# Kernel tuning notes

Hardware: AMD Instinct MI355X
Metric: run time of the kernel (lower is better)

## Reference

```python
import jax, jax.numpy as jnp
import numpy as np

B, S, HID = 2, 2048, 2048
H, KV, D = 16, 4, 128
EPS = 1e-6


def rms_norm(x, w, eps=EPS):
    # Qwen3.5 convention: (1 + weight) * RMSNorm(x), weight init 0
    v = jnp.mean(x * x, axis=-1, keepdims=True)
    return (1.0 + w) * (x * jax.lax.rsqrt(v + eps))


def rotate_half(x):
    x1, x2 = jnp.split(x, 2, axis=-1)
    return jnp.concatenate([-x2, x1], axis=-1)


def apply_rope(x, cos, sin):
    # x: [B,S,h,D]; cos/sin: [S,D]
    c = cos[None, :, None, :]
    s = sin[None, :, None, :]
    return x * c + rotate_half(x) * s


def setup_inputs():
    key = jax.random.key(0)
    ks = jax.random.split(key, 8)
    sc = 0.02
    hidden_states = jax.random.normal(ks[0], (B, S, HID), jnp.float32)
    past_key_value = jnp.zeros((B, 2, KV, S, D), jnp.float32)
    pos = jnp.arange(S, dtype=jnp.float32)
    inv_freq = 1.0 / (10000.0 ** (jnp.arange(0, D, 2, dtype=jnp.float32) / D))
    ang = pos[:, None] * inv_freq[None, :]                    # [S, D/2]
    cos = jnp.concatenate([jnp.cos(ang), jnp.cos(ang)], -1)   # [S, D]
    sin = jnp.concatenate([jnp.sin(ang), jnp.sin(ang)], -1)
    rope_rotary_cos_sin = jnp.stack([cos, sin], axis=1)       # [S, 2, D]
    context_lengths = jnp.full((B,), S, dtype=jnp.int32)
    kvcache_start_index = jnp.zeros((B,), dtype=jnp.int32)
    Wq = jax.random.normal(ks[1], (HID, H * D * 2), jnp.float32) * sc
    Wk = jax.random.normal(ks[2], (HID, KV * D), jnp.float32) * sc
    Wv = jax.random.normal(ks[3], (HID, KV * D), jnp.float32) * sc
    Wo = jax.random.normal(ks[4], (H * D, HID), jnp.float32) * sc
    q_norm_w = jax.random.normal(ks[5], (D,), jnp.float32) * sc
    k_norm_w = jax.random.normal(ks[6], (D,), jnp.float32) * sc
    return {"hidden_states": hidden_states, "past_key_value": past_key_value,
            "rope_rotary_cos_sin": rope_rotary_cos_sin,
            "context_lengths": context_lengths,
            "kvcache_start_index": kvcache_start_index,
            "Wq": Wq, "Wk": Wk, "Wv": Wv, "Wo": Wo,
            "q_norm_w": q_norm_w, "k_norm_w": k_norm_w}


def reference(hidden_states, past_key_value, rope_rotary_cos_sin,
              context_lengths, kvcache_start_index,
              Wq, Wk, Wv, Wo, q_norm_w, k_norm_w):
    # projections
    q_out = jnp.einsum('bsc,cd->bsd', hidden_states, Wq).reshape(B, S, H, 2 * D)
    query, gate = jnp.split(q_out, 2, axis=-1)                # each [B,S,H,D]
    k = jnp.einsum('bsc,cd->bsd', hidden_states, Wk).reshape(B, S, KV, D)
    v = jnp.einsum('bsc,cd->bsd', hidden_states, Wv).reshape(B, S, KV, D)
    # per-head QK RMSNorm
    query = rms_norm(query, q_norm_w)
    k = rms_norm(k, k_norm_w)
    # RoPE
    cos, sin = rope_rotary_cos_sin[:, 0, :], rope_rotary_cos_sin[:, 1, :]
    query = apply_rope(query, cos, sin)
    k = apply_rope(k, cos, sin)
    # write KV cache (prefill at start index 0)
    present = past_key_value.at[:, 0, :, :S, :].set(jnp.transpose(k, (0, 2, 1, 3)))
    present = present.at[:, 1, :, :S, :].set(jnp.transpose(v, (0, 2, 1, 3)))
    # GQA causal attention
    group = H // KV
    k_r = jnp.repeat(k, group, axis=2)                        # [B,S,H,D]
    v_r = jnp.repeat(v, group, axis=2)
    scores = jnp.einsum('bqhd,bkhd->bhqk', query, k_r) / jnp.sqrt(jnp.float32(D))
    causal = jnp.tril(jnp.ones((S, S), dtype=bool))
    scores = jnp.where(causal[None, None], scores, jnp.float32(-1e30))
    probs = jax.nn.softmax(scores, axis=-1)
    attn = jnp.einsum('bhqk,bkhd->bqhd', probs, v_r)          # [B,S,H,D]
    # sigmoid gating + output proj
    attn = attn * jax.nn.sigmoid(gate)
    out = jnp.einsum('bsd,dc->bsc', attn.reshape(B, S, H * D), Wo)
    return out, present
```

## Files before the change

kernel.cpp:

```cpp
#include <hip/hip_runtime.h>
#include <hip/hip_bf16.h>
#include <cstdint>
#include <cstddef>

#define BB   2
#define SS   2048
#define HIDD 2048
#define HH   16
#define KVH  4
#define DD   128
#define NQKV 5120
#define MM   4096

typedef unsigned short u16t;
typedef __attribute__((ext_vector_type(8))) short s16x8;
typedef __attribute__((ext_vector_type(4))) short s16x4;
typedef __attribute__((ext_vector_type(4))) float f32x4;

__device__ __forceinline__ u16t f2bf(float f) {
  unsigned u = __float_as_uint(f);
  u += 0x7fffu + ((u >> 16) & 1u);
  return (u16t)(u >> 16);
}
__device__ __forceinline__ float bf2f(u16t h) {
  return __uint_as_float(((unsigned)h) << 16);
}
__device__ __forceinline__ void gload_lds16(const void* g, void* l) {
  __builtin_amdgcn_global_load_lds(
      (const __attribute__((address_space(1))) unsigned int*)g,
      (__attribute__((address_space(3))) unsigned int*)l, 16, 0, 0);
}
__device__ __forceinline__ unsigned cvtpk_bf16(float lo, float hi) {
  unsigned r;
  asm("v_cvt_pk_bf16_f32 %0, %1, %2" : "=v"(r) : "v"(lo), "v"(hi));
  return r;
}
__device__ __forceinline__ f32x4 fmax4(f32x4 a, f32x4 b) {
  f32x4 r;
  r[0] = fmaxf(a[0], b[0]); r[1] = fmaxf(a[1], b[1]);
  r[2] = fmaxf(a[2], b[2]); r[3] = fmaxf(a[3], b[3]);
  return r;
}

__global__ __launch_bounds__(256) void prep_all(const float* __restrict__ hidden,
                                                const float* __restrict__ Wq,
                                                const float* __restrict__ Wk,
                                                const float* __restrict__ Wv,
                                                const float* __restrict__ Wo,
                                                u16t* __restrict__ Xb,
                                                u16t* __restrict__ Wt,
                                                u16t* __restrict__ Wot) {
  __shared__ float lds[64 * 65];
  int bid = blockIdx.x;
  int t = threadIdx.x;
  if (bid < 8192) {
    size_t i = ((size_t)bid * 256 + t) * 4;
    f32x4 v = *(const f32x4*)(hidden + i);
    s16x4 o;
    o[0] = (short)f2bf(v[0]); o[1] = (short)f2bf(v[1]);
    o[2] = (short)f2bf(v[2]); o[3] = (short)f2bf(v[3]);
    *(s16x4*)(Xb + i) = o;
    return;
  }
  bid -= 8192;
  const float* src; u16t* dst; int N;
  if (bid < 2048)      { src = Wq; dst = Wt;                         N = 4096; }
  else if (bid < 2304) { src = Wk; dst = Wt + (size_t)4096 * HIDD;   N = 512;  bid -= 2048; }
  else if (bid < 2560) { src = Wv; dst = Wt + (size_t)4608 * HIDD;   N = 512;  bid -= 2304; }
  else                 { src = Wo; dst = Wot;                        N = 2048; bid -= 2560; }
  const int ktiles = HIDD / 64;
  int n0 = (bid / ktiles) << 6;
  int k0 = (bid % ktiles) << 6;
#pragma unroll
  for (int i = 0; i < 16; i++) {
    int idx = i * 256 + t;
    int r = idx >> 6, c = idx & 63;
    lds[c * 65 + r] = src[(size_t)(k0 + r) * N + n0 + c];
  }
  __syncthreads();
#pragma unroll
  for (int i = 0; i < 16; i++) {
    int idx = i * 256 + t;
    int rr = idx >> 6, kk = idx & 63;
    dst[(size_t)(n0 + rr) * HIDD + k0 + kk] = f2bf(lds[rr * 65 + kk]);
  }
}

__device__ __forceinline__ s16x8 ldsfrag(const char* half, int r, int g) {
  return *(const s16x8*)(half + r * 64 + ((g ^ ((r >> 1) & 3)) << 4));
}
__device__ __forceinline__ void stage_half(char* ldsbase, const u16t* gbase,
                                           int K, int kcol, int tid) {
#pragma unroll
  for (int i = 0; i < 2; i++) {
    int o16 = i * 512 + tid;
    int r = o16 >> 2;
    int cs = (o16 & 3) ^ ((r >> 1) & 3);
    gload_lds16(gbase + (size_t)r * K + kcol + cs * 8, ldsbase + o16 * 16);
  }
}

template <typename CT>
__global__ __launch_bounds__(512, 2) void gemm8(const u16t* __restrict__ A,
                                                const u16t* __restrict__ Bt,
                                                CT* __restrict__ C,
                                                int M, int N, int K) {
  extern __shared__ __align__(16) char lds[];
  char* As = lds;
  char* Bs = lds + 65536;
  int tid = threadIdx.x, lane = tid & 63, w = tid >> 6;
  int wm = w >> 2, wn = w & 3;
  int cpx = gridDim.x >> 3;
  int wgid = (blockIdx.x & 7) * cpx + (blockIdx.x >> 3);
  int bm = wgid & 15, bn = wgid >> 4;
  int m0 = bm << 8, n0 = bn << 8;
  const u16t* Ag = A + (size_t)m0 * K;
  const u16t* Bg = Bt + (size_t)n0 * K;
  const int NT = K >> 6;

  stage_half(As, Ag, K, 0, tid);
  stage_half(Bs, Bg, K, 0, tid);
  stage_half(As + 16384, Ag, K, 32, tid);
  stage_half(Bs + 16384, Bg, K, 32, tid);
  stage_half(As + 32768, Ag, K, 64, tid);
  stage_half(Bs + 32768, Bg, K, 64, tid);
  asm volatile("s_waitcnt vmcnt(8)" ::: "memory");
  __builtin_amdgcn_s_barrier();

  const f32x4 fz = {0.f, 0.f, 0.f, 0.f};
  f32x4 acc[8][4];
#pragma unroll
  for (int i = 0; i < 8; i++)
#pragma unroll
    for (int j = 0; j < 4; j++) acc[i][j] = fz;
  s16x8 afr[4], bfr[4];
  int g = lane >> 4;
  int rA = (lane & 15) + wm * 128;
  int rB = (lane & 15) + wn * 64;

  for (int kt = 0; kt < NT; kt++) {
    int cur = kt & 1;
    char* Acur = As + cur * 32768;
    char* Bcur = Bs + cur * 32768;
    char* Anxt = As + (cur ^ 1) * 32768;
    char* Bnxt = Bs + (cur ^ 1) * 32768;
#pragma unroll
    for (int ni = 0; ni < 4; ni++) bfr[ni] = ldsfrag(Bcur, rB + ni * 16, g);
#pragma unroll
    for (int mi = 0; mi < 4; mi++) afr[mi] = ldsfrag(Acur, rA + mi * 16, g);
    if (kt + 1 < NT) stage_half(Anxt + 16384, Ag, K, (kt + 1) * 64 + 32, tid);
    __builtin_amdgcn_s_barrier();
    asm volatile("s_waitcnt lgkmcnt(0)" ::: "memory");
    __builtin_amdgcn_s_setprio(1);
#pragma unroll
    for (int mi = 0; mi < 4; mi++)
#pragma unroll
      for (int ni = 0; ni < 4; ni++)
        acc[mi][ni] = __builtin_amdgcn_mfma_f32_16x16x32_bf16(afr[mi], bfr[ni], acc[mi][ni], 0, 0, 0);
    __builtin_amdgcn_s_setprio(0);
    __builtin_amdgcn_s_barrier();
#pragma unroll
    for (int mi = 0; mi < 4; mi++) afr[mi] = ldsfrag(Acur, rA + 64 + mi * 16, g);
    if (kt + 1 < NT) stage_half(Bnxt + 16384, Bg, K, (kt + 1) * 64 + 32, tid);
    __builtin_amdgcn_s_barrier();
    asm volatile("s_waitcnt lgkmcnt(0)" ::: "memory");
    __builtin_amdgcn_s_setprio(1);
#pragma unroll
    for (int mi = 0; mi < 4; mi++)
#pragma unroll
      for (int ni = 0; ni < 4; ni++)
        acc[4 + mi][ni] = __builtin_amdgcn_mfma_f32_16x16x32_bf16(afr[mi], bfr[ni], acc[4 + mi][ni], 0, 0, 0);
    __builtin_amdgcn_s_setprio(0);
    if (kt + 1 < NT) asm volatile("s_waitcnt vmcnt(8)" ::: "memory");
    else             asm volatile("s_waitcnt vmcnt(0)" ::: "memory");
    __builtin_amdgcn_s_barrier();
#pragma unroll
    for (int ni = 0; ni < 4; ni++) bfr[ni] = ldsfrag(Bcur + 16384, rB + ni * 16, g);
#pragma unroll
    for (int mi = 0; mi < 4; mi++) afr[mi] = ldsfrag(Acur + 16384, rA + mi * 16, g);
    if (kt + 2 < NT) stage_half(Acur, Ag, K, (kt + 2) * 64, tid);
    __builtin_amdgcn_s_barrier();
    asm volatile("s_waitcnt lgkmcnt(0)" ::: "memory");
    __builtin_amdgcn_s_setprio(1);
#pragma unroll
    for (int mi = 0; mi < 4; mi++)
#pragma unroll
      for (int ni = 0; ni < 4; ni++)
        acc[mi][ni] = __builtin_amdgcn_mfma_f32_16x16x32_bf16(afr[mi], bfr[ni], acc[mi][ni], 0, 0, 0);
    __builtin_amdgcn_s_setprio(0);
    __builtin_amdgcn_s_barrier();
#pragma unroll
    for (int mi = 0; mi < 4; mi++) afr[mi] = ldsfrag(Acur + 16384, rA + 64 + mi * 16, g);
    if (kt + 2 < NT) stage_half(Bcur, Bg, K, (kt + 2) * 64, tid);
    __builtin_amdgcn_s_barrier();
    asm volatile("s_waitcnt lgkmcnt(0)" ::: "memory");
    __builtin_amdgcn_s_setprio(1);
#pragma unroll
    for (int mi = 0; mi < 4; mi++)
#pragma unroll
      for (int ni = 0; ni < 4; ni++)
        acc[4 + mi][ni] = __builtin_amdgcn_mfma_f32_16x16x32_bf16(afr[mi], bfr[ni], acc[4 + mi][ni], 0, 0, 0);
    __builtin_amdgcn_s_setprio(0);
    if (kt < NT - 1) {
      if (kt + 2 < NT) asm volatile("s_waitcnt vmcnt(8)" ::: "memory");
      else             asm volatile("s_waitcnt vmcnt(4)" ::: "memory");
    }
    __builtin_amdgcn_s_barrier();
  }
#pragma unroll
  for (int mi = 0; mi < 8; mi++)
#pragma unroll
    for (int ni = 0; ni < 4; ni++) {
      int row0 = m0 + wm * 128 + mi * 16 + ((lane >> 4) << 2);
      int col = n0 + wn * 64 + ni * 16 + (lane & 15);
#pragma unroll
      for (int j = 0; j < 4; j++) {
        if constexpr (sizeof(CT) == 2)
          C[(size_t)(row0 + j) * N + col] = f2bf(acc[mi][ni][j]);
        else
          C[(size_t)(row0 + j) * N + col] = acc[mi][ni][j];
      }
    }
}

template <typename CT>
__global__ __launch_bounds__(256) void gemm_bt(const u16t* __restrict__ A,
                                               const u16t* __restrict__ Bt,
                                               CT* __restrict__ C,
                                               int M, int N, int K) {
  __shared__ __align__(16) char As[128 * 64];
  __shared__ __align__(16) char Bs[128 * 64];
  int tid = threadIdx.x;
  int lane = tid & 63;
  int w = tid >> 6;
  int cpx = gridDim.x >> 3;
  int wgid = ((int)blockIdx.x & 7) * cpx + ((int)blockIdx.x >> 3);
  int mtiles = M >> 7;
  int bm = wgid % mtiles;
  int bn = wgid / mtiles;
  int m0 = bm << 7, n0 = bn << 7;
  int wr = (w >> 1) * 64, wc = (w & 1) * 64;

  const f32x4 fz = {0.f, 0.f, 0.f, 0.f};
  f32x4 acc[4][4];
#pragma unroll
  for (int i = 0; i < 4; i++)
#pragma unroll
    for (int j = 0; j < 4; j++) acc[i][j] = fz;

  for (int k0 = 0; k0 < K; k0 += 32) {
    __syncthreads();
#pragma unroll
    for (int i = 0; i < 2; i++) {
      int idx = i * 256 + tid;
      int r = idx >> 2, c = idx & 3;
      int csrc = c ^ ((r >> 1) & 3);
      gload_lds16(A + (size_t)(m0 + r) * K + k0 + csrc * 8, As + idx * 16);
      gload_lds16(Bt + (size_t)(n0 + r) * K + k0 + csrc * 8, Bs + idx * 16);
    }
    __syncthreads();
    s16x8 af[4], bf[4];
    int g = lane >> 4;
#pragma unroll
    for (int mi = 0; mi < 4; mi++) {
      int r = wr + mi * 16 + (lane & 15);
      af[mi] = *(const s16x8*)(As + r * 64 + ((g ^ ((r >> 1) & 3)) << 4));
    }
#pragma unroll
    for (int ni = 0; ni < 4; ni++) {
      int r = wc + ni * 16 + (lane & 15);
      bf[ni] = *(const s16x8*)(Bs + r * 64 + ((g ^ ((r >> 1) & 3)) << 4));
    }
#pragma unroll
    for (int mi = 0; mi < 4; mi++)
#pragma unroll
      for (int ni = 0; ni < 4; ni++)
        acc[mi][ni] = __builtin_amdgcn_mfma_f32_16x16x32_bf16(af[mi], bf[ni], acc[mi][ni], 0, 0, 0);
  }
#pragma unroll
  for (int mi = 0; mi < 4; mi++)
#pragma unroll
    for (int ni = 0; ni < 4; ni++) {
      int row0 = m0 + wr + mi * 16 + ((lane >> 4) << 2);
      int col = n0 + wc + ni * 16 + (lane & 15);
#pragma unroll
      for (int j = 0; j < 4; j++) {
        if constexpr (sizeof(CT) == 2)
          C[(size_t)(row0 + j) * N + col] = f2bf(acc[mi][ni][j]);
        else
          C[(size_t)(row0 + j) * N + col] = acc[mi][ni][j];
      }
    }
}

__global__ __launch_bounds__(256) void qk_norm_rope(const u16t* __restrict__ Cqkv,
                                                    const float* __restrict__ rope,
                                                    const float* __restrict__ qw,
                                                    const float* __restrict__ kw,
                                                    u16t* __restrict__ Qb,
                                                    u16t* __restrict__ Kb,
                                                    u16t* __restrict__ Gs,
                                                    float* __restrict__ present) {
  int wid = blockIdx.x * 4 + (threadIdx.x >> 6);
  int lane = threadIdx.x & 63;
  const int NQ = BB * SS * HH;
  if (wid < NQ) {
    int b = wid >> 15;
    int rem = wid & 32767;
    int s = rem >> 4, h = rem & 15;
    const u16t* base = Cqkv + (size_t)(b * SS + s) * NQKV + h * 256;
    float xlo = bf2f(base[lane]), xhi = bf2f(base[64 + lane]);
    float ss = xlo * xlo + xhi * xhi;
    ss += __shfl_xor(ss, 1);  ss += __shfl_xor(ss, 2);  ss += __shfl_xor(ss, 4);
    ss += __shfl_xor(ss, 8);  ss += __shfl_xor(ss, 16); ss += __shfl_xor(ss, 32);
    float r = rsqrtf(ss * (1.f / 128.f) + 1e-6f);
    float qlo = xlo * r * (1.f + qw[lane]);
    float qhi = xhi * r * (1.f + qw[64 + lane]);
    const float* cs = rope + (size_t)s * 256;
    float clo = cs[lane], chi = cs[64 + lane];
    float slo = cs[128 + lane], shi = cs[192 + lane];
    const float SC = 0.08838834764831845f * 1.4426950408889634f;
    float olo = (qlo * clo - qhi * slo) * SC;
    float ohi = (qhi * chi + qlo * shi) * SC;
    size_t qoff = (((size_t)b * HH + h) * SS + s) * DD;
    Qb[qoff + lane] = f2bf(olo);
    Qb[qoff + 64 + lane] = f2bf(ohi);
    float glo = bf2f(base[128 + lane]), ghi = bf2f(base[192 + lane]);
    size_t goff = ((size_t)(b * SS + s)) * (HH * DD) + h * DD;
    Gs[goff + lane] = f2bf(1.f / (1.f + __expf(-glo)));
    Gs[goff + 64 + lane] = f2bf(1.f / (1.f + __expf(-ghi)));
  } else {
    int wid2 = wid - NQ;
    int b = wid2 >> 13;
    int rem = wid2 & 8191;
    int s = rem >> 2, kv = rem & 3;
    const u16t* base = Cqkv + (size_t)(b * SS + s) * NQKV + 4096 + kv * 128;
    float xlo = bf2f(base[lane]), xhi = bf2f(base[64 + lane]);
    float ss = xlo * xlo + xhi * xhi;
    ss += __shfl_xor(ss, 1);  ss += __shfl_xor(ss, 2);  ss += __shfl_xor(ss, 4);
    ss += __shfl_xor(ss, 8);  ss += __shfl_xor(ss, 16); ss += __shfl_xor(ss, 32);
    float r = rsqrtf(ss * (1.f / 128.f) + 1e-6f);
    float klo = xlo * r * (1.f + kw[lane]);
    float khi = xhi * r * (1.f + kw[64 + lane]);
    const float* cs = rope + (size_t)s * 256;
    float clo = cs[lane], chi = cs[64 + lane];
    float slo = cs[128 + lane], shi = cs[192 + lane];
    float olo = klo * clo - khi * slo;
    float ohi = khi * chi + klo * shi;
    size_t koff = (((size_t)b * KVH + kv) * SS + s) * DD;
    Kb[koff + lane] = f2bf(olo);
    Kb[koff + 64 + lane] = f2bf(ohi);
    size_t poff = (((size_t)(b * 2 * KVH + kv)) * SS + s) * DD;
    present[poff + lane] = olo;
    present[poff + 64 + lane] = ohi;
  }
}

__global__ __launch_bounds__(256) void v_write(const u16t* __restrict__ Cqkv,
                                               float* __restrict__ present,
                                               u16t* __restrict__ Vtb) {
  __shared__ float lds[128 * 65];
  int t = threadIdx.x;
  int b = blockIdx.x >> 7;
  int kv = (blockIdx.x >> 5) & 3;
  int s0 = (blockIdx.x & 31) << 6;
#pragma unroll
  for (int i = 0; i < 32; i++) {
    int idx = i * 256 + t;
    int sp = idx >> 7, d = idx & 127;
    float v = bf2f(Cqkv[(size_t)(b * SS + s0 + sp) * NQKV + 4608 + kv * 128 + d]);
    present[(((size_t)(b * 2 * KVH + KVH + kv)) * SS + s0 + sp) * DD + d] = v;
    lds[d * 65 + sp] = v;
  }
  __syncthreads();
#pragma unroll
  for (int i = 0; i < 8; i++) {
    int d = i * 16 + (t >> 4);
    int sp = (t & 15) * 4;
    s16x4 pk;
    pk[0] = (short)f2bf(lds[d * 65 + sp + 0]);
    pk[1] = (short)f2bf(lds[d * 65 + sp + 1]);
    pk[2] = (short)f2bf(lds[d * 65 + sp + 2]);
    pk[3] = (short)f2bf(lds[d * 65 + sp + 3]);
    *(s16x4*)(Vtb + ((size_t)(b * KVH + kv) * DD + d) * SS + s0 + sp) = pk;
  }
}

__global__ __launch_bounds__(256) void attn_kernel(const u16t* __restrict__ Qb,
                                                   const u16t* __restrict__ Kb,
                                                   const u16t* __restrict__ Vtb,
                                                   const u16t* __restrict__ Gs,
                                                   u16t* __restrict__ AttG) {
  __shared__ __align__(16) char Ks[2][16384];
  __shared__ __align__(16) char Vs[2][16384];
  __shared__ __align__(16) char Ps[4 * 2048];

  int tid = threadIdx.x, lane = tid & 63, w = tid >> 6;
  int x = blockIdx.x & 7;
  int b = x >> 2, kv = x & 3;
  int rr = blockIdx.x >> 3;
  int h = kv * 4 + (rr & 3);
  int p = rr >> 2;

  const u16t* Kbase = Kb + (((size_t)(b * KVH + kv)) * SS) * DD;
  const u16t* Vbase = Vtb + (((size_t)(b * KVH + kv)) * DD) * SS;

  auto stageK = [&](int kt, int buf) {
#pragma unroll
    for (int i = 0; i < 4; i++) {
      int idx = i * 256 + tid;
      int r_ = idx >> 4, c_ = idx & 15;
      gload_lds16(Kbase + (size_t)(kt * 64 + r_) * DD + (c_ ^ (r_ & 7)) * 8, Ks[buf] + idx * 16);
    }
  };
  auto stageV = [&](int kt, int buf) {
#pragma unroll
    for (int i = 0; i < 4; i++) {
      int idx = i * 256 + tid;
      int r_ = idx >> 3, c_ = idx & 7;
      gload_lds16(Vbase + (size_t)r_ * SS + kt * 64 + (c_ ^ (r_ & 7)) * 8, Vs[buf] + idx * 16);
    }
  };

  const f32x4 fz = {0.f, 0.f, 0.f, 0.f};
  int g = lane >> 4;
  int q15 = lane & 15;
  int q7 = q15 & 7;
  char* pq = Ps + w * 2048 + q15 * 128;
  int cur = 0;

  stageK(0, 0);
  stageV(0, 0);

  for (int seg = 0; seg < 2; seg++) {
    int qt = (seg == 0) ? (31 - p) : p;
    const u16t* Qbase = Qb + (((size_t)(b * HH + h)) * SS + qt * 64) * DD;
    s16x8 qf[4];
    {
      const u16t* qrow = Qbase + (size_t)(w * 16 + q15) * DD + g * 8;
#pragma unroll
      for (int ks = 0; ks < 4; ks++) qf[ks] = *(const s16x8*)(qrow + ks * 32);
    }
    f32x4 acco[8];
#pragma unroll
    for (int f = 0; f < 8; f++) acco[f] = fz;
    float mrun = -INFINITY, lrun = 0.f;

    if (seg == 0) {
      asm volatile("s_waitcnt vmcnt(0)" ::: "memory");
      __builtin_amdgcn_s_barrier();
    }

    for (int kt = 0; kt <= qt; kt++) {
      bool havenext = (kt < qt) || (seg == 0);
      if (havenext) {
        int nk = (kt < qt) ? (kt + 1) : 0;
        stageK(nk, cur ^ 1);
        stageV(nk, cur ^ 1);
      }
      f32x4 accs[4];
#pragma unroll
      for (int ni = 0; ni < 4; ni++) accs[ni] = fz;
#pragma unroll
      for (int ni = 0; ni < 4; ni++) {
        int r = ni * 16 + q15;
#pragma unroll
        for (int ks = 0; ks < 4; ks++) {
          int g2 = ks * 4 + g;
          s16x8 bfk = *(const s16x8*)(Ks[cur] + r * 256 + ((g2 ^ (r & 7)) << 4));
          accs[ni] = __builtin_amdgcn_mfma_f32_16x16x32_bf16(bfk, qf[ks], accs[ni], 0, 0, 0);
        }
      }
      if (kt == qt) {
        int ql = w * 16 + q15;
#pragma unroll
        for (int ni = 0; ni < 4; ni++)
#pragma unroll
          for (int j = 0; j < 4; j++) {
            int kl = ni * 16 + (g << 2) + j;
            if (kl > ql) accs[ni][j] = -1e30f;
          }
      }
      f32x4 m4 = fmax4(fmax4(accs[0], accs[1]), fmax4(accs[2], accs[3]));
      float mt = fmaxf(fmaxf(m4[0], m4[1]), fmaxf(m4[2], m4[3]));
      mt = fmaxf(mt, __shfl_xor(mt, 16));
      mt = fmaxf(mt, __shfl_xor(mt, 32));
      float mnew = fmaxf(mrun, mt);
      float alpha = __builtin_amdgcn_exp2f(mrun - mnew);
      mrun = mnew;
#pragma unroll
      for (int ni = 0; ni < 4; ni++)
#pragma unroll
        for (int j = 0; j < 4; j++)
          accs[ni][j] = __builtin_amdgcn_exp2f(accs[ni][j] - mnew);
      f32x4 s01 = accs[0] + accs[1];
      f32x4 s23 = accs[2] + accs[3];
      f32x4 s4 = s01 + s23;
      float rs = (s4[0] + s4[1]) + (s4[2] + s4[3]);
      rs += __shfl_xor(rs, 16);
      rs += __shfl_xor(rs, 32);
      lrun = lrun * alpha + rs;
      float ar[4];
#pragma unroll
      for (int j = 0; j < 4; j++) ar[j] = __shfl(alpha, (g << 2) + j);
#pragma unroll
      for (int f = 0; f < 8; f++)
#pragma unroll
        for (int j = 0; j < 4; j++) acco[f][j] *= ar[j];

#pragma unroll
      for (int ni = 0; ni < 4; ni++) {
        uint2 pk;
        pk.x = cvtpk_bf16(accs[ni][0], accs[ni][1]);
        pk.y = cvtpk_bf16(accs[ni][2], accs[ni][3]);
        int gr = ni * 2 + (g >> 1);
        *(uint2*)(pq + ((gr ^ q7) << 4) + ((g & 1) << 3)) = pk;
      }
#pragma unroll
      for (int ks2 = 0; ks2 < 2; ks2++) {
        s16x8 pa = *(const s16x8*)(pq + (((ks2 * 4 + g) ^ q7) << 4));
#pragma unroll
        for (int f = 0; f < 8; f++) {
          int d = f * 16 + q15;
          s16x8 vf = *(const s16x8*)(Vs[cur] + d * 128 + (((ks2 * 4 + g) ^ (d & 7)) << 4));
          acco[f] = __builtin_amdgcn_mfma_f32_16x16x32_bf16(pa, vf, acco[f], 0, 0, 0);
        }
      }
      if (havenext) {
        asm volatile("s_waitcnt vmcnt(0)" ::: "memory");
        __builtin_amdgcn_s_barrier();
        cur ^= 1;
      }
    }
    float lr[4];
#pragma unroll
    for (int j = 0; j < 4; j++) lr[j] = __shfl(lrun, (g << 2) + j);
#pragma unroll
    for (int f = 0; f < 8; f++) {
      int d = f * 16 + q15;
#pragma unroll
      for (int j = 0; j < 4; j++) {
        int srow = qt * 64 + w * 16 + (g << 2) + j;
        float o = acco[f][j] / lr[j];
        size_t off = ((size_t)b * SS + srow) * (HH * DD) + h * DD + d;
        float gt = bf2f(Gs[off]);
        AttG[off] = f2bf(o * gt);
      }
    }
  }
}

extern "C" void kernel_launch(void* const* d_in, const int* in_sizes, int n_in,
                              void* d_out, int out_size, void* d_ws, size_t ws_size,
                              hipStream_t stream) {
  const float* hidden = (const float*)d_in[0];
  const float* rope   = (const float*)d_in[2];
  const float* Wq     = (const float*)d_in[5];
  const float* Wk     = (const float*)d_in[6];
  const float* Wv     = (const float*)d_in[7];
  const float* Wo     = (const float*)d_in[8];
  const float* qw     = (const float*)d_in[9];
  const float* kw     = (const float*)d_in[10];
  float* out = (float*)d_out;
  float* present = out + (size_t)BB * SS * HIDD;

  char* ws = (char*)d_ws;
  u16t* Xb    = (u16t*)(ws);
  u16t* Wt    = (u16t*)(ws + 16777216);
  u16t* Wot   = (u16t*)(ws + 37748736);
  u16t* Cqkv  = (u16t*)(ws + 46137344);
  u16t* Qb    = (u16t*)(ws + 88080384);
  u16t* Kb    = (u16t*)(ws + 104857600);
  u16t* Vtb   = (u16t*)(ws + 109051904);
  u16t* Gs    = (u16t*)(ws + 113246208);
  u16t* AttG  = Xb;

  (void)hipFuncSetAttribute(reinterpret_cast<const void*>(gemm8<u16t>),
                            hipFuncAttributeMaxDynamicSharedMemorySize, 131072);
  (void)hipFuncSetAttribute(reinterpret_cast<const void*>(gemm8<float>),
                            hipFuncAttributeMaxDynamicSharedMemorySize, 131072);

  prep_all<<<8192 + 3584, 256, 0, stream>>>(hidden, Wq, Wk, Wv, Wo, Xb, Wt, Wot);
  gemm8<u16t><<<(MM / 256) * (4096 / 256), 512, 131072, stream>>>(Xb, Wt, Cqkv, MM, NQKV, HIDD);
  gemm_bt<u16t><<<(MM / 128) * (1024 / 128), 256, 0, stream>>>(
      Xb, Wt + (size_t)4096 * HIDD, Cqkv + 4096, MM, NQKV, HIDD);
  qk_norm_rope<<<(BB * SS * (HH + KVH)) / 4, 256, 0, stream>>>(Cqkv, rope, qw, kw, Qb, Kb, Gs, present);
  v_write<<<BB * KVH * (SS / 64), 256, 0, stream>>>(Cqkv, present, Vtb);
  attn_kernel<<<BB * HH * (SS / 128), 256, 0, stream>>>(Qb, Kb, Vtb, Gs, AttG);
  gemm8<float><<<(MM / 256) * (HIDD / 256), 512, 131072, stream>>>(AttG, Wot, out, MM, HIDD, HIDD);
}
```

Measured before the change: 289.0 us.

## Parametrize gemm8 tile width, use 256x128 tiles for output projection, tune attention

The 8-wave GEMM is now templated on the N tile width, with the LDS layout, load counts and vmcnt waits derived from it. The output projection uses 256x128 tiles, so 128 workgroups become 256 and fill more of the CUs, at the cost of less operand reuse per tile. The attention kernel gets launch_bounds(256,2) and precomputes its swizzled LDS offsets outside the loop, which removes per-iteration address arithmetic but holds more values in registers.

```diff
diff --git a/kernel.cpp b/kernel.cpp
--- a/kernel.cpp
+++ b/kernel.cpp
@@ -40,6 +40,15 @@
   r[0] = fmaxf(a[0], b[0]); r[1] = fmaxf(a[1], b[1]);
   r[2] = fmaxf(a[2], b[2]); r[3] = fmaxf(a[3], b[3]);
   return r;
+}
+template <int N>
+__device__ __forceinline__ void waitvm() {
+  static_assert(N == 0 || N == 3 || N == 4 || N == 6 || N == 8, "add literal");
+  if constexpr (N == 0)      asm volatile("s_waitcnt vmcnt(0)" ::: "memory");
+  else if constexpr (N == 3) asm volatile("s_waitcnt vmcnt(3)" ::: "memory");
+  else if constexpr (N == 4) asm volatile("s_waitcnt vmcnt(4)" ::: "memory");
+  else if constexpr (N == 6) asm volatile("s_waitcnt vmcnt(6)" ::: "memory");
+  else if constexpr (N == 8) asm volatile("s_waitcnt vmcnt(8)" ::: "memory");
 }
 
 __global__ __launch_bounds__(256) void prep_all(const float* __restrict__ hidden,
@@ -89,10 +98,11 @@
 __device__ __forceinline__ s16x8 ldsfrag(const char* half, int r, int g) {
   return *(const s16x8*)(half + r * 64 + ((g ^ ((r >> 1) & 3)) << 4));
 }
+template <int NL>
 __device__ __forceinline__ void stage_half(char* ldsbase, const u16t* gbase,
                                            int K, int kcol, int tid) {
 #pragma unroll
-  for (int i = 0; i < 2; i++) {
+  for (int i = 0; i < NL; i++) {
     int o16 = i * 512 + tid;
     int r = o16 >> 2;
     int cs = (o16 & 3) ^ ((r >> 1) & 3);
@@ -100,119 +110,124 @@
   }
 }
 
-template <typename CT>
+template <int BN, typename CT>
 __global__ __launch_bounds__(512, 2) void gemm8(const u16t* __restrict__ A,
                                                 const u16t* __restrict__ Bt,
                                                 CT* __restrict__ C,
                                                 int M, int N, int K) {
+  constexpr int NLB = BN / 128;
+  constexpr int AHALF = 16384, ASLOT = 32768;
+  constexpr int BHALF = BN * 64, BSLOT = 2 * BHALF;
+  constexpr int PAIR = 2 + NLB;
+  constexpr int NI = BN / 64;
   extern __shared__ __align__(16) char lds[];
   char* As = lds;
-  char* Bs = lds + 65536;
+  char* Bs = lds + 2 * ASLOT;
   int tid = threadIdx.x, lane = tid & 63, w = tid >> 6;
   int wm = w >> 2, wn = w & 3;
   int cpx = gridDim.x >> 3;
   int wgid = (blockIdx.x & 7) * cpx + (blockIdx.x >> 3);
   int bm = wgid & 15, bn = wgid >> 4;
-  int m0 = bm << 8, n0 = bn << 8;
+  int m0 = bm << 8, n0 = bn * BN;
   const u16t* Ag = A + (size_t)m0 * K;
   const u16t* Bg = Bt + (size_t)n0 * K;
   const int NT = K >> 6;
 
-  stage_half(As, Ag, K, 0, tid);
-  stage_half(Bs, Bg, K, 0, tid);
-  stage_half(As + 16384, Ag, K, 32, tid);
-  stage_half(Bs + 16384, Bg, K, 32, tid);
-  stage_half(As + 32768, Ag, K, 64, tid);
-  stage_half(Bs + 32768, Bg, K, 64, tid);
-  asm volatile("s_waitcnt vmcnt(8)" ::: "memory");
+  stage_half<2>(As, Ag, K, 0, tid);
+  stage_half<NLB>(Bs, Bg, K, 0, tid);
+  stage_half<2>(As + AHALF, Ag, K, 32, tid);
+  stage_half<NLB>(Bs + BHALF, Bg, K, 32, tid);
+  stage_half<2>(As + ASLOT, Ag, K, 64, tid);
+  stage_half<NLB>(Bs + BSLOT, Bg, K, 64, tid);
+  waitvm<2 * PAIR>();
   __builtin_amdgcn_s_barrier();
 
   const f32x4 fz = {0.f, 0.f, 0.f, 0.f};
-  f32x4 acc[8][4];
+  f32x4 acc[8][NI];
 #pragma unroll
   for (int i = 0; i < 8; i++)
 #pragma unroll
-    for (int j = 0; j < 4; j++) acc[i][j] = fz;
-  s16x8 afr[4], bfr[4];
+    for (int j = 0; j < NI; j++) acc[i][j] = fz;
+  s16x8 afr[4], bfr[NI];
   int g = lane >> 4;
   int rA = (lane & 15) + wm * 128;
-  int rB = (lane & 15) + wn * 64;
+  int rB = (lane & 15) + wn * (BN / 4);
 
   for (int kt = 0; kt < NT; kt++) {
     int cur = kt & 1;
-    char* Acur = As + cur * 32768;
-    char* Bcur = Bs + cur * 32768;
-    char* Anxt = As + (cur ^ 1) * 32768;
-    char* Bnxt = Bs + (cur ^ 1) * 32768;
-#pragma unroll
-    for (int ni = 0; ni < 4; ni++) bfr[ni] = ldsfrag(Bcur, rB + ni * 16, g);
+    char* Acur = As + cur * ASLOT;
+    char* Bcur = Bs + cur * BSLOT;
+    char* Anxt = As + (cur ^ 1) * ASLOT;
+    char* Bnxt = Bs + (cur ^ 1) * BSLOT;
+#pragma unroll
+    for (int ni = 0; ni < NI; ni++) bfr[ni] = ldsfrag(Bcur, rB + ni * 16, g);
 #pragma unroll
     for (int mi = 0; mi < 4; mi++) afr[mi] = ldsfrag(Acur, rA + mi * 16, g);
-    if (kt + 1 < NT) stage_half(Anxt + 16384, Ag, K, (kt + 1) * 64 + 32, tid);
+    if (kt + 1 < NT) stage_half<2>(Anxt + AHALF, Ag, K, (kt + 1) * 64 + 32, tid);
     __builtin_amdgcn_s_barrier();
     asm volatile("s_waitcnt lgkmcnt(0)" ::: "memory");
     __builtin_amdgcn_s_setprio(1);
 #pragma unroll
     for (int mi = 0; mi < 4; mi++)
 #pragma unroll
-      for (int ni = 0; ni < 4; ni++)
+      for (int ni = 0; ni < NI; ni++)
         acc[mi][ni] = __builtin_amdgcn_mfma_f32_16x16x32_bf16(afr[mi], bfr[ni], acc[mi][ni], 0, 0, 0);
     __builtin_amdgcn_s_setprio(0);
     __builtin_amdgcn_s_barrier();
 #pragma unroll
     for (int mi = 0; mi < 4; mi++) afr[mi] = ldsfrag(Acur, rA + 64 + mi * 16, g);
-    if (kt + 1 < NT) stage_half(Bnxt + 16384, Bg, K, (kt + 1) * 64 + 32, tid);
+    if (kt + 1 < NT) stage_half<NLB>(Bnxt + BHALF, Bg, K, (kt + 1) * 64 + 32, tid);
     __builtin_amdgcn_s_barrier();
     asm volatile("s_waitcnt lgkmcnt(0)" ::: "memory");
     __builtin_amdgcn_s_setprio(1);
 #pragma unroll
     for (int mi = 0; mi < 4; mi++)
 #pragma unroll
-      for (int ni = 0; ni < 4; ni++)
+      for (int ni = 0; ni < NI; ni++)
         acc[4 + mi][ni] = __builtin_amdgcn_mfma_f32_16x16x32_bf16(afr[mi], bfr[ni], acc[4 + mi][ni], 0, 0, 0);
     __builtin_amdgcn_s_setprio(0);
-    if (kt + 1 < NT) asm volatile("s_waitcnt vmcnt(8)" ::: "memory");
-    else             asm volatile("s_waitcnt vmcnt(0)" ::: "memory");
-    __builtin_amdgcn_s_barrier();
-#pragma unroll
-    for (int ni = 0; ni < 4; ni++) bfr[ni] = ldsfrag(Bcur + 16384, rB + ni * 16, g);
-#pragma unroll
-    for (int mi = 0; mi < 4; mi++) afr[mi] = ldsfrag(Acur + 16384, rA + mi * 16, g);
-    if (kt + 2 < NT) stage_half(Acur, Ag, K, (kt + 2) * 64, tid);
+    if (kt + 1 < NT) waitvm<2 * PAIR>();
+    else             waitvm<0>();
+    __builtin_amdgcn_s_barrier();
+#pragma unroll
+    for (int ni = 0; ni < NI; ni++) bfr[ni] = ldsfrag(Bcur + BHALF, rB + ni * 16, g);
+#pragma unroll
+    for (int mi = 0; mi < 4; mi++) afr[mi] = ldsfrag(Acur + AHALF, rA + mi * 16, g);
+    if (kt + 2 < NT) stage_half<2>(Acur, Ag, K, (kt + 2) * 64, tid);
     __builtin_amdgcn_s_barrier();
     asm volatile("s_waitcnt lgkmcnt(0)" ::: "memory");
     __builtin_amdgcn_s_setprio(1);
 #pragma unroll
     for (int mi = 0; mi < 4; mi++)
 #pragma unroll
-      for (int ni = 0; ni < 4; ni++)
+      for (int ni = 0; ni < NI; ni++)
         acc[mi][ni] = __builtin_amdgcn_mfma_f32_16x16x32_bf16(afr[mi], bfr[ni], acc[mi][ni], 0, 0, 0);
     __builtin_amdgcn_s_setprio(0);
     __builtin_amdgcn_s_barrier();
 #pragma unroll
-    for (int mi = 0; mi < 4; mi++) afr[mi] = ldsfrag(Acur + 16384, rA + 64 + mi * 16, g);
-    if (kt + 2 < NT) stage_half(Bcur, Bg, K, (kt + 2) * 64, tid);
+    for (int mi = 0; mi < 4; mi++) afr[mi] = ldsfrag(Acur + AHALF, rA + 64 + mi * 16, g);
+    if (kt + 2 < NT) stage_half<NLB>(Bcur, Bg, K, (kt + 2) * 64, tid);
     __builtin_amdgcn_s_barrier();
     asm volatile("s_waitcnt lgkmcnt(0)" ::: "memory");
     __builtin_amdgcn_s_setprio(1);
 #pragma unroll
     for (int mi = 0; mi < 4; mi++)
 #pragma unroll
-      for (int ni = 0; ni < 4; ni++)
+      for (int ni = 0; ni < NI; ni++)
         acc[4 + mi][ni] = __builtin_amdgcn_mfma_f32_16x16x32_bf16(afr[mi], bfr[ni], acc[4 + mi][ni], 0, 0, 0);
     __builtin_amdgcn_s_setprio(0);
     if (kt < NT - 1) {
-      if (kt + 2 < NT) asm volatile("s_waitcnt vmcnt(8)" ::: "memory");
-      else             asm volatile("s_waitcnt vmcnt(4)" ::: "memory");
+      if (kt + 2 < NT) waitvm<2 * PAIR>();
+      else             waitvm<PAIR>();
     }
     __builtin_amdgcn_s_barrier();
   }
 #pragma unroll
   for (int mi = 0; mi < 8; mi++)
 #pragma unroll
-    for (int ni = 0; ni < 4; ni++) {
+    for (int ni = 0; ni < NI; ni++) {
       int row0 = m0 + wm * 128 + mi * 16 + ((lane >> 4) << 2);
-      int col = n0 + wn * 64 + ni * 16 + (lane & 15);
+      int col = n0 + wn * (BN / 4) + ni * 16 + (lane & 15);
 #pragma unroll
       for (int j = 0; j < 4; j++) {
         if constexpr (sizeof(CT) == 2)
@@ -386,13 +401,13 @@
   }
 }
 
-__global__ __launch_bounds__(256) void attn_kernel(const u16t* __restrict__ Qb,
-                                                   const u16t* __restrict__ Kb,
-                                                   const u16t* __restrict__ Vtb,
-                                                   const u16t* __restrict__ Gs,
-                                                   u16t* __restrict__ AttG) {
-  __shared__ __align__(16) char Ks[2][16384];
-  __shared__ __align__(16) char Vs[2][16384];
+__global__ __launch_bounds__(256, 2) void attn_kernel(const u16t* __restrict__ Qb,
+                                                      const u16t* __restrict__ Kb,
+                                                      const u16t* __restrict__ Vtb,
+                                                      const u16t* __restrict__ Gs,
+                                                      u16t* __restrict__ AttG) {
+  __shared__ __align__(16) char Ks[2 * 16384];
+  __shared__ __align__(16) char Vs[2 * 16384];
   __shared__ __align__(16) char Ps[4 * 2048];
 
   int tid = threadIdx.x, lane = tid & 63, w = tid >> 6;
@@ -410,7 +425,8 @@
     for (int i = 0; i < 4; i++) {
       int idx = i * 256 + tid;
       int r_ = idx >> 4, c_ = idx & 15;
-      gload_lds16(Kbase + (size_t)(kt * 64 + r_) * DD + (c_ ^ (r_ & 7)) * 8, Ks[buf] + idx * 16);
+      gload_lds16(Kbase + (size_t)(kt * 64 + r_) * DD + (c_ ^ (r_ & 7)) * 8,
+                  Ks + buf * 16384 + idx * 16);
     }
   };
   auto stageV = [&](int kt, int buf) {
@@ -418,7 +434,8 @@
     for (int i = 0; i < 4; i++) {
       int idx = i * 256 + tid;
       int r_ = idx >> 3, c_ = idx & 7;
-      gload_lds16(Vbase + (size_t)r_ * SS + kt * 64 + (c_ ^ (r_ & 7)) * 8, Vs[buf] + idx * 16);
+      gload_lds16(Vbase + (size_t)r_ * SS + kt * 64 + (c_ ^ (r_ & 7)) * 8,
+                  Vs + buf * 16384 + idx * 16);
     }
   };
 
@@ -429,6 +446,26 @@
   char* pq = Ps + w * 2048 + q15 * 128;
   int cur = 0;
 
+  int ka[4][4];
+#pragma unroll
+  for (int ni = 0; ni < 4; ni++)
+#pragma unroll
+    for (int ks = 0; ks < 4; ks++)
+      ka[ni][ks] = (ni * 16 + q15) * 256 + (((ks * 4 + g) ^ q7) << 4);
+  int va[2][8];
+#pragma unroll
+  for (int ks2 = 0; ks2 < 2; ks2++)
+#pragma unroll
+    for (int f = 0; f < 8; f++)
+      va[ks2][f] = (f * 16 + q15) * 128 + (((ks2 * 4 + g) ^ q7) << 4);
+  int pr_[2];
+#pragma unroll
+  for (int ks2 = 0; ks2 < 2; ks2++) pr_[ks2] = ((ks2 * 4 + g) ^ q7) << 4;
+  int pw_[4];
+#pragma unroll
+  for (int ni = 0; ni < 4; ni++)
+    pw_[ni] = (((ni * 2 + (g >> 1)) ^ q7) << 4) + ((g & 1) << 3);
+
   stageK(0, 0);
   stageV(0, 0);
 
@@ -458,19 +495,18 @@
         stageK(nk, cur ^ 1);
         stageV(nk, cur ^ 1);
       }
+      const char* kc = Ks + (cur << 14);
+      const char* vc = Vs + (cur << 14);
       f32x4 accs[4];
 #pragma unroll
       for (int ni = 0; ni < 4; ni++) accs[ni] = fz;
 #pragma unroll
-      for (int ni = 0; ni < 4; ni++) {
-        int r = ni * 16 + q15;
+      for (int ni = 0; ni < 4; ni++)
 #pragma unroll
         for (int ks = 0; ks < 4; ks++) {
-          int g2 = ks * 4 + g;
-          s16x8 bfk = *(const s16x8*)(Ks[cur] + r * 256 + ((g2 ^ (r & 7)) << 4));
+          s16x8 bfk = *(const s16x8*)(kc + ka[ni][ks]);
           accs[ni] = __builtin_amdgcn_mfma_f32_16x16x32_bf16(bfk, qf[ks], accs[ni], 0, 0, 0);
         }
-      }
       if (kt == qt) {
         int ql = w * 16 + q15;
 #pragma unroll
@@ -493,9 +529,7 @@
 #pragma unroll
         for (int j = 0; j < 4; j++)
           accs[ni][j] = __builtin_amdgcn_exp2f(accs[ni][j] - mnew);
-      f32x4 s01 = accs[0] + accs[1];
-      f32x4 s23 = accs[2] + accs[3];
-      f32x4 s4 = s01 + s23;
+      f32x4 s4 = (accs[0] + accs[1]) + (accs[2] + accs[3]);
       float rs = (s4[0] + s4[1]) + (s4[2] + s4[3]);
       rs += __shfl_xor(rs, 16);
       rs += __shfl_xor(rs, 32);
@@ -513,16 +547,14 @@
         uint2 pk;
         pk.x = cvtpk_bf16(accs[ni][0], accs[ni][1]);
         pk.y = cvtpk_bf16(accs[ni][2], accs[ni][3]);
-        int gr = ni * 2 + (g >> 1);
-        *(uint2*)(pq + ((gr ^ q7) << 4) + ((g & 1) << 3)) = pk;
+        *(uint2*)(pq + pw_[ni]) = pk;
       }
 #pragma unroll
       for (int ks2 = 0; ks2 < 2; ks2++) {
-        s16x8 pa = *(const s16x8*)(pq + (((ks2 * 4 + g) ^ q7) << 4));
+        s16x8 pa = *(const s16x8*)(pq + pr_[ks2]);
 #pragma unroll
         for (int f = 0; f < 8; f++) {
-          int d = f * 16 + q15;
-          s16x8 vf = *(const s16x8*)(Vs[cur] + d * 128 + (((ks2 * 4 + g) ^ (d & 7)) << 4));
+          s16x8 vf = *(const s16x8*)(vc + va[ks2][f]);
           acco[f] = __builtin_amdgcn_mfma_f32_16x16x32_bf16(pa, vf, acco[f], 0, 0, 0);
         }
       }
@@ -575,17 +607,17 @@
   u16t* Gs    = (u16t*)(ws + 113246208);
   u16t* AttG  = Xb;
 
-  (void)hipFuncSetAttribute(reinterpret_cast<const void*>(gemm8<u16t>),
+  (void)hipFuncSetAttribute(reinterpret_cast<const void*>(gemm8<256, u16t>),
                             hipFuncAttributeMaxDynamicSharedMemorySize, 131072);
-  (void)hipFuncSetAttribute(reinterpret_cast<const void*>(gemm8<float>),
-                            hipFuncAttributeMaxDynamicSharedMemorySize, 131072);
+  (void)hipFuncSetAttribute(reinterpret_cast<const void*>(gemm8<128, float>),
+                            hipFuncAttributeMaxDynamicSharedMemorySize, 98304);
 
   prep_all<<<8192 + 3584, 256, 0, stream>>>(hidden, Wq, Wk, Wv, Wo, Xb, Wt, Wot);
-  gemm8<u16t><<<(MM / 256) * (4096 / 256), 512, 131072, stream>>>(Xb, Wt, Cqkv, MM, NQKV, HIDD);
+  gemm8<256, u16t><<<(MM / 256) * (4096 / 256), 512, 131072, stream>>>(Xb, Wt, Cqkv, MM, NQKV, HIDD);
   gemm_bt<u16t><<<(MM / 128) * (1024 / 128), 256, 0, stream>>>(
       Xb, Wt + (size_t)4096 * HIDD, Cqkv + 4096, MM, NQKV, HIDD);
   qk_norm_rope<<<(BB * SS * (HH + KVH)) / 4, 256, 0, stream>>>(Cqkv, rope, qw, kw, Qb, Kb, Gs, present);
   v_write<<<BB * KVH * (SS / 64), 256, 0, stream>>>(Cqkv, present, Vtb);
   attn_kernel<<<BB * HH * (SS / 128), 256, 0, stream>>>(Qb, Kb, Vtb, Gs, AttG);
-  gemm8<float><<<(MM / 256) * (HIDD / 256), 512, 131072, stream>>>(AttG, Wot, out, MM, HIDD, HIDD);
-}
+  gemm8<128, float><<<(MM / 256) * (HIDD / 128), 512, 98304, stream>>>(AttG, Wot, out, MM, HIDD, HIDD);
+}
```

After: 266.1 us. -7.9%, faster.
